# Performance work log

Hardware: AMD Instinct MI355X
Metric: run time of the kernel (lower is better)

Reference implementation:

```python
import jax, jax.numpy as jnp
import numpy as np

GROUPS = 32
EPS = 1e-5
HEAD_DIM = 64


def group_norm(x, gamma, beta):
    # x: [B, L, C]; normalize over (L, C//G) within each of G channel groups
    B, L, C = x.shape
    g = x.reshape(B, L, GROUPS, C // GROUPS)
    mean = g.mean(axis=(1, 3), keepdims=True)
    var = g.var(axis=(1, 3), keepdims=True)
    g = (g - mean) * jax.lax.rsqrt(var + EPS)
    return g.reshape(B, L, C) * gamma + beta


def setup_inputs() -> dict:
    key = jax.random.key(0)
    ks = jax.random.split(key, 4)
    B, H, W, C = 16, 32, 32, 512
    x = jax.random.normal(ks[0], (B, H, W, C), dtype=jnp.float32)
    timesteps = jax.random.randint(ks[1], (B,), 0, 1000)
    gamma = jnp.ones((C,), jnp.float32)
    beta = jnp.zeros((C,), jnp.float32)
    w_qkv = jax.random.normal(ks[2], (C, 3 * C), dtype=jnp.float32) * (1.0 / np.sqrt(C))
    b_qkv = jnp.zeros((3 * C,), jnp.float32)
    w_out = jax.random.normal(ks[3], (C, C), dtype=jnp.float32) * (1.0 / np.sqrt(C))
    b_out = jnp.zeros((C,), jnp.float32)
    return {"x": x, "timesteps": timesteps, "gamma": gamma, "beta": beta,
            "w_qkv": w_qkv, "b_qkv": b_qkv, "w_out": w_out, "b_out": b_out}


def reference(x, timesteps, gamma, beta, w_qkv, b_qkv, w_out, b_out):
    B, H, W, C = x.shape
    L = H * W
    nh = C // HEAD_DIM
    factor = jnp.asarray(1.0 / np.sqrt(np.sqrt(HEAD_DIM)), x.dtype)  # applied to both q and k

    xf = x.reshape(B, L, C)
    qkv = group_norm(xf, gamma, beta) @ w_qkv + b_qkv        # [B, L, 3C]
    q, k, v = jnp.split(qkv, 3, axis=-1)

    def heads(t):  # [B, L, C] -> [B, nh, L, d]
        return t.reshape(B, L, nh, HEAD_DIM).transpose(0, 2, 1, 3)

    q, k, v = heads(q) * factor, heads(k) * factor, heads(v)
    scores = jnp.einsum('bhqd,bhkd->bhqk', q, k)             # [B, nh, L, L]
    attn = jax.nn.softmax(scores, axis=-1)
    out = jnp.einsum('bhqk,bhkd->bhqd', attn, v)             # [B, nh, L, d]
    out = out.transpose(0, 2, 1, 3).reshape(B, L, C)
    h = out @ w_out + b_out
    return (xf + h).reshape(B, H, W, C)
```

## Files before the change

### kernel.cpp

```cpp
#include <hip/hip_runtime.h>

#define Bn 16
#define Ln 1024
#define Cn 512
#define Mn (Bn*Ln)
#define N3n 1536

typedef unsigned short u16;
typedef __attribute__((ext_vector_type(8))) short short8;
typedef __attribute__((ext_vector_type(4))) float f32x4;
typedef __attribute__((ext_vector_type(16))) float f32x16;

typedef const __attribute__((address_space(1))) void* gas_p;
typedef __attribute__((address_space(3))) void* las_p;

__device__ inline void gl_lds16(const void* g, void* l) {
  __builtin_amdgcn_global_load_lds((gas_p)g, (las_p)l, 16, 0, 0);
}

__device__ inline u16 f2bf(float f) {
  union { float f; unsigned u; } v; v.f = f;
  unsigned r = v.u + 0x7FFFu + ((v.u >> 16) & 1u);
  return (u16)(r >> 16);
}

__device__ inline unsigned pk2(float a, float b) {
  return (__float_as_uint(a) >> 16) | (__float_as_uint(b) & 0xFFFF0000u);
}

__device__ inline f32x4 mfma16(short8 a, short8 b, f32x4 c) {
  return __builtin_amdgcn_mfma_f32_16x16x32_bf16(a, b, c, 0, 0, 0);
}
__device__ inline f32x16 mfma32(short8 a, short8 b, f32x16 c) {
  return __builtin_amdgcn_mfma_f32_32x32x16_bf16(a, b, c, 0, 0, 0);
}

__global__ __launch_bounds__(256) void k_gn(const float* __restrict__ x,
                                            const float* __restrict__ gamma,
                                            const float* __restrict__ beta,
                                            u16* __restrict__ gn) {
  __shared__ __attribute__((aligned(16))) float xs[1024 * 16];
  __shared__ float red[8];
  __shared__ float stat[2];
  int bid = blockIdx.x;
  int b = bid >> 5, g = bid & 31;
  const float* base = x + (size_t)b * (Ln * Cn) + g * 16;
  int tid = threadIdx.x;
  int c = tid & 3;
  float s1 = 0.f, s2 = 0.f;
  for (int i = 0; i < 16; ++i) {
    int s = i * 256 + tid;
    int r = s >> 2;
    float4 v = *(const float4*)(base + (size_t)r * Cn + c * 4);
    *(float4*)(xs + (size_t)s * 4) = v;
    s1 += v.x + v.y + v.z + v.w;
    s2 += v.x * v.x + v.y * v.y + v.z * v.z + v.w * v.w;
  }
  s1 += __shfl_xor(s1, 1);  s2 += __shfl_xor(s2, 1);
  s1 += __shfl_xor(s1, 2);  s2 += __shfl_xor(s2, 2);
  s1 += __shfl_xor(s1, 4);  s2 += __shfl_xor(s2, 4);
  s1 += __shfl_xor(s1, 8);  s2 += __shfl_xor(s2, 8);
  s1 += __shfl_xor(s1, 16); s2 += __shfl_xor(s2, 16);
  s1 += __shfl_xor(s1, 32); s2 += __shfl_xor(s2, 32);
  int w = tid >> 6, lane = tid & 63;
  if (lane == 0) { red[w] = s1; red[4 + w] = s2; }
  __syncthreads();
  if (tid == 0) {
    float a = red[0] + red[1] + red[2] + red[3];
    float q = red[4] + red[5] + red[6] + red[7];
    float mean = a * (1.f / 16384.f);
    float var = q * (1.f / 16384.f) - mean * mean;
    stat[0] = mean;
    stat[1] = rsqrtf(var + 1e-5f);
  }
  __syncthreads();
  float mean = stat[0], rstd = stat[1];
  float4 gv = *(const float4*)(gamma + g * 16 + c * 4);
  float4 bv = *(const float4*)(beta + g * 16 + c * 4);
  u16* gdst = gn + (size_t)b * (Ln * Cn) + g * 16;
  for (int i = 0; i < 16; ++i) {
    int s = i * 256 + tid;
    int r = s >> 2;
    float4 v = *(const float4*)(xs + (size_t)s * 4);
    ushort4 o;
    o.x = f2bf((v.x - mean) * rstd * gv.x + bv.x);
    o.y = f2bf((v.y - mean) * rstd * gv.y + bv.y);
    o.z = f2bf((v.z - mean) * rstd * gv.z + bv.z);
    o.w = f2bf((v.w - mean) * rstd * gv.w + bv.w);
    *(ushort4*)(gdst + (size_t)r * Cn + c * 4) = o;
  }
}

__global__ __launch_bounds__(256) void k_wtrans(const float* __restrict__ wqkv,
                                                const float* __restrict__ wout,
                                                u16* __restrict__ wqkvT,
                                                u16* __restrict__ woutT) {
  __shared__ float T[64][65];
  int bid = blockIdx.x;
  const float* src; u16* dst; int srcN, k0, n0;
  if (bid < 192) {
    src = wqkv; dst = wqkvT; srcN = 1536;
    int nt = bid % 24, kt = bid / 24;
    n0 = nt * 64; k0 = kt * 64;
  } else {
    int b2 = bid - 192;
    src = wout; dst = woutT; srcN = 512;
    int nt = b2 & 7, kt = b2 >> 3;
    n0 = nt * 64; k0 = kt * 64;
  }
  int tid = threadIdx.x;
  int r = tid >> 4, c4 = tid & 15;
#pragma unroll
  for (int i = 0; i < 4; ++i) {
    int rr = i * 16 + r;
    float4 v = *(const float4*)(src + (size_t)(k0 + rr) * srcN + n0 + c4 * 4);
    T[rr][c4 * 4 + 0] = v.x; T[rr][c4 * 4 + 1] = v.y;
    T[rr][c4 * 4 + 2] = v.z; T[rr][c4 * 4 + 3] = v.w;
  }
  __syncthreads();
  int r2 = tid >> 3, c2 = tid & 7;
#pragma unroll
  for (int i = 0; i < 2; ++i) {
    int nn = i * 32 + r2;
    int kk = c2 * 8;
    uint4 pk;
    pk.x = (unsigned)f2bf(T[kk + 0][nn]) | ((unsigned)f2bf(T[kk + 1][nn]) << 16);
    pk.y = (unsigned)f2bf(T[kk + 2][nn]) | ((unsigned)f2bf(T[kk + 3][nn]) << 16);
    pk.z = (unsigned)f2bf(T[kk + 4][nn]) | ((unsigned)f2bf(T[kk + 5][nn]) << 16);
    pk.w = (unsigned)f2bf(T[kk + 6][nn]) | ((unsigned)f2bf(T[kk + 7][nn]) << 16);
    *(uint4*)(dst + (size_t)(n0 + nn) * 512 + k0 + kk) = pk;
  }
}

__global__ __launch_bounds__(256) void k_qkv(const u16* __restrict__ gn,
                                             const u16* __restrict__ wT,
                                             const float* __restrict__ bias,
                                             u16* __restrict__ qb,
                                             u16* __restrict__ kb,
                                             u16* __restrict__ vT) {
  __shared__ __attribute__((aligned(16))) char smem[66560];
  int bid = blockIdx.x;
  int wg = (bid & 7) * 192 + (bid >> 3);
  int tn = wg % 12, tm = wg / 12;
  int m0 = tm * 128, n0 = tn * 128;
  int tid = threadIdx.x;
  int w = tid >> 6, lane = tid & 63, lr = lane & 15, lg = lane >> 4;
  int wr = w >> 1, wc = w & 1;
  const f32x4 fzero = {0.f, 0.f, 0.f, 0.f};
  f32x4 acc[4][4];
#pragma unroll
  for (int mi = 0; mi < 4; ++mi)
#pragma unroll
    for (int ni = 0; ni < 4; ++ni) acc[mi][ni] = fzero;

#pragma unroll
  for (int i = 0; i < 4; ++i) {
    int s = i * 256 + tid;
    int r = s >> 3, c = s & 7;
    gl_lds16(gn + ((size_t)(m0 + r) * 512 + ((c ^ (r & 7)) << 3)),
             smem + ((s & ~63) << 4));
    gl_lds16(wT + ((size_t)(n0 + r) * 512 + ((c ^ (r & 7)) << 3)),
             smem + 32768 + ((s & ~63) << 4));
  }
  __syncthreads();

  for (int kt = 0; kt < 8; ++kt) {
    int cur = kt & 1;
    char* Asb = smem + cur * 16384;
    char* Bsb = smem + 32768 + cur * 16384;
    if (kt < 7) {
      int nb = cur ^ 1, k0n = (kt + 1) * 64;
#pragma unroll
      for (int i = 0; i < 4; ++i) {
        int s = i * 256 + tid;
        int r = s >> 3, c = s & 7;
        gl_lds16(gn + ((size_t)(m0 + r) * 512 + k0n + ((c ^ (r & 7)) << 3)),
                 smem + nb * 16384 + ((s & ~63) << 4));
        gl_lds16(wT + ((size_t)(n0 + r) * 512 + k0n + ((c ^ (r & 7)) << 3)),
                 smem + 32768 + nb * 16384 + ((s & ~63) << 4));
      }
    }
#pragma unroll
    for (int ks = 0; ks < 2; ++ks) {
      short8 af[4], bf[4];
#pragma unroll
      for (int mi = 0; mi < 4; ++mi) {
        int row = wr * 64 + mi * 16 + lr;
        int ck = ks * 4 + lg;
        af[mi] = *(const short8*)(Asb + row * 128 + ((ck ^ (lr & 7)) << 4));
      }
#pragma unroll
      for (int ni = 0; ni < 4; ++ni) {
        int row = wc * 64 + ni * 16 + lr;
        int ck = ks * 4 + lg;
        bf[ni] = *(const short8*)(Bsb + row * 128 + ((ck ^ (lr & 7)) << 4));
      }
#pragma unroll
      for (int mi = 0; mi < 4; ++mi)
#pragma unroll
        for (int ni = 0; ni < 4; ++ni)
          acc[mi][ni] = mfma16(af[mi], bf[ni], acc[mi][ni]);
    }
    __syncthreads();
  }

  if (tn >= 8) {
    float* T = (float*)smem;
#pragma unroll
    for (int mi = 0; mi < 4; ++mi)
#pragma unroll
      for (int ni = 0; ni < 4; ++ni) {
        int n_l = wc * 64 + ni * 16 + lr;
        float bn = bias[n0 + n_l];
#pragma unroll
        for (int rr = 0; rr < 4; ++rr) {
          int m_l = wr * 64 + mi * 16 + lg * 4 + rr;
          T[n_l * 130 + m_l] = acc[mi][ni][rr] + bn;
        }
      }
    __syncthreads();
    int n_l = tid >> 1, half = tid & 1;
    int nv = n0 - 1024 + n_l;
    int h = nv >> 6, dd = nv & 63;
    int bb = m0 >> 10, li0 = m0 & 1023;
    u16* dst = vT + ((size_t)(bb * 8 + h) * 64 + dd) * 1024 + li0;
    const float* Tr = T + n_l * 130;
#pragma unroll
    for (int j = 0; j < 8; ++j) {
      int mb = half * 8 + 16 * j;
#define SIG(IDX) (((IDX) & ~15) | (((IDX) & 4) << 1) | (((IDX) & 8) >> 1) | ((IDX) & 3))
      uint4 o;
      o.x = (unsigned)f2bf(Tr[SIG(mb + 0)]) | ((unsigned)f2bf(Tr[SIG(mb + 1)]) << 16);
      o.y = (unsigned)f2bf(Tr[SIG(mb + 2)]) | ((unsigned)f2bf(Tr[SIG(mb + 3)]) << 16);
      o.z = (unsigned)f2bf(Tr[SIG(mb + 4)]) | ((unsigned)f2bf(Tr[SIG(mb + 5)]) << 16);
      o.w = (unsigned)f2bf(Tr[SIG(mb + 6)]) | ((unsigned)f2bf(Tr[SIG(mb + 7)]) << 16);
#undef SIG
      *(uint4*)(dst + mb) = o;
    }
  } else {
    const float C1 = 0.18033688011112042f;
#pragma unroll
    for (int mi = 0; mi < 4; ++mi) {
#pragma unroll
      for (int ni = 0; ni < 4; ++ni) {
        int n = n0 + wc * 64 + ni * 16 + lr;
        float bn = bias[n];
        int which = n >> 9, nn = n & 511;
        int h = nn >> 6, dd = nn & 63;
#pragma unroll
        for (int rr = 0; rr < 4; ++rr) {
          int m = m0 + wr * 64 + mi * 16 + lg * 4 + rr;
          float v = acc[mi][ni][rr] + bn;
          int bb = m >> 10, li = m & 1023;
          if (which == 0)
            qb[((size_t)(bb * 8 + h) * 1024 + li) * 64 + dd] = f2bf(v * C1);
          else
            kb[((size_t)(bb * 8 + h) * 1024 + li) * 64 + dd] = f2bf(v);
        }
      }
    }
  }
}

__global__ __launch_bounds__(512, 4) void k_attn(const u16* __restrict__ qb,
                                                 const u16* __restrict__ kb,
                                                 const u16* __restrict__ vT,
                                                 u16* __restrict__ ob) {
  __shared__ __attribute__((aligned(16))) u16 Ks[3 * 64 * 64];
  __shared__ __attribute__((aligned(16))) u16 Vs[3 * 64 * 64];
  int bid = blockIdx.x;
  int xq = bid & 7, kk = bid >> 3;
  int bh = ((kk & 15) << 3) | xq;
  int qt = kk >> 4;
  const u16* qh = qb + (size_t)bh * 65536;
  const u16* kh = kb + (size_t)bh * 65536;
  const u16* vh = vT + (size_t)bh * 65536;
  int tid = threadIdx.x, w = tid >> 6, lane = tid & 63;
  int l31 = lane & 31, lhi = lane >> 5;
  int q0 = qt * 256 + w * 32;

  short8 qf[4];
#pragma unroll
  for (int ks = 0; ks < 4; ++ks)
    qf[ks] = *(const short8*)(qh + (size_t)(q0 + l31) * 64 + ks * 16 + lhi * 8);

  f32x16 accO[2];
#pragma unroll
  for (int dt = 0; dt < 2; ++dt)
#pragma unroll
    for (int r = 0; r < 16; ++r) accO[dt][r] = 0.f;
  float lst = 0.f;

  int sr = tid >> 3, sc8 = tid & 7;
  size_t koff = (size_t)sr * 64 + ((sc8 ^ (sr & 7)) << 3);
  size_t voff = (size_t)sr * 1024 + ((sc8 ^ (sr & 7)) << 3);
  int ldst = (tid & ~63) << 4;

  gl_lds16(kh + koff, (char*)Ks + ldst);
  gl_lds16(vh + voff, (char*)Vs + ldst);
  gl_lds16(kh + 4096 + koff, (char*)Ks + 8192 + ldst);
  gl_lds16(vh + 64 + voff, (char*)Vs + 8192 + ldst);
  asm volatile("s_waitcnt vmcnt(2)" ::: "memory");
  __builtin_amdgcn_s_barrier();

#pragma unroll 1
  for (int jt = 0; jt < 16; ++jt) {
    int cb = jt % 3;
    char* Ksb = (char*)Ks + cb * 8192;
    char* Vsb = (char*)Vs + cb * 8192;
    if (jt < 14) {
      int nb = (jt + 2) % 3;
      gl_lds16(kh + (size_t)(jt + 2) * 4096 + koff, (char*)Ks + nb * 8192 + ldst);
      gl_lds16(vh + (size_t)(jt + 2) * 64 + voff, (char*)Vs + nb * 8192 + ldst);
    }

    f32x16 sc0, sc1;
#pragma unroll
    for (int r = 0; r < 16; ++r) { sc0[r] = 0.f; sc1[r] = 0.f; }
#pragma unroll
    for (int ks = 0; ks < 4; ++ks) {
      int row = l31;
      short8 kf = *(const short8*)(Ksb + row * 128 + (((2 * ks + lhi) ^ (row & 7)) << 4));
      sc0 = mfma32(kf, qf[ks], sc0);
    }
#pragma unroll
    for (int ks = 0; ks < 4; ++ks) {
      int row = 32 + l31;
      short8 kf = *(const short8*)(Ksb + row * 128 + (((2 * ks + lhi) ^ (row & 7)) << 4));
      sc1 = mfma32(kf, qf[ks], sc1);
    }

    float rs = 0.f;
#pragma unroll
    for (int r = 0; r < 16; ++r) {
      float pp = __builtin_amdgcn_exp2f(sc0[r]);
      sc0[r] = pp; rs += pp;
    }
#pragma unroll
    for (int r = 0; r < 16; ++r) {
      float pp = __builtin_amdgcn_exp2f(sc1[r]);
      sc1[r] = pp; rs += pp;
    }
    lst += rs;

    short8 ap[4];
    {
      union { uint4 u; short8 s; } cv;
      cv.u.x = pk2(sc0[0], sc0[1]);  cv.u.y = pk2(sc0[2], sc0[3]);
      cv.u.z = pk2(sc0[4], sc0[5]);  cv.u.w = pk2(sc0[6], sc0[7]);
      ap[0] = cv.s;
      cv.u.x = pk2(sc0[8], sc0[9]);  cv.u.y = pk2(sc0[10], sc0[11]);
      cv.u.z = pk2(sc0[12], sc0[13]); cv.u.w = pk2(sc0[14], sc0[15]);
      ap[1] = cv.s;
      cv.u.x = pk2(sc1[0], sc1[1]);  cv.u.y = pk2(sc1[2], sc1[3]);
      cv.u.z = pk2(sc1[4], sc1[5]);  cv.u.w = pk2(sc1[6], sc1[7]);
      ap[2] = cv.s;
      cv.u.x = pk2(sc1[8], sc1[9]);  cv.u.y = pk2(sc1[10], sc1[11]);
      cv.u.z = pk2(sc1[12], sc1[13]); cv.u.w = pk2(sc1[14], sc1[15]);
      ap[3] = cv.s;
    }

#pragma unroll
    for (int ks2 = 0; ks2 < 4; ++ks2) {
#pragma unroll
      for (int dt = 0; dt < 2; ++dt) {
        int row = dt * 32 + l31;
        short8 bv = *(const short8*)(Vsb + row * 128 + (((2 * ks2 + lhi) ^ (row & 7)) << 4));
        accO[dt] = mfma32(ap[ks2], bv, accO[dt]);
      }
    }

    if (jt < 14)
      asm volatile("s_waitcnt vmcnt(2)" ::: "memory");
    else
      asm volatile("s_waitcnt vmcnt(0)" ::: "memory");
    __builtin_amdgcn_s_barrier();
  }

  int b = bh >> 3, h = bh & 7;
  float lt = lst + __shfl_xor(lst, 32);
  float il = 1.f / lt;
#pragma unroll
  for (int reg = 0; reg < 16; ++reg) {
    int qrow = (reg & 3) + 8 * (reg >> 2) + 4 * lhi;
    float ib = __shfl(il, qrow);
    int row = q0 + qrow;
#pragma unroll
    for (int dt = 0; dt < 2; ++dt) {
      int col = h * 64 + dt * 32 + l31;
      ob[(size_t)(b * 1024 + row) * 512 + col] = f2bf(accO[dt][reg] * ib);
    }
  }
}

__global__ __launch_bounds__(256) void k_out(const u16* __restrict__ ob,
                                             const u16* __restrict__ wT,
                                             const float* __restrict__ bias,
                                             const float* __restrict__ x,
                                             float* __restrict__ out) {
  __shared__ __attribute__((aligned(16))) u16 As[2 * 128 * 64];
  __shared__ __attribute__((aligned(16))) u16 Bs[2 * 128 * 64];
  int bid = blockIdx.x;
  int wg = (bid & 7) * 64 + (bid >> 3);
  int tn = wg & 3, tm = wg >> 2;
  int m0 = tm * 128, n0 = tn * 128;
  int tid = threadIdx.x;
  int w = tid >> 6, lane = tid & 63, lr = lane & 15, lg = lane >> 4;
  int wr = w >> 1, wc = w & 1;
  const f32x4 fzero = {0.f, 0.f, 0.f, 0.f};
  f32x4 acc[4][4];
#pragma unroll
  for (int mi = 0; mi < 4; ++mi)
#pragma unroll
    for (int ni = 0; ni < 4; ++ni) acc[mi][ni] = fzero;

#pragma unroll
  for (int i = 0; i < 4; ++i) {
    int s = i * 256 + tid;
    int r = s >> 3, c = s & 7;
    gl_lds16(ob + ((size_t)(m0 + r) * 512 + ((c ^ (r & 7)) << 3)),
             (char*)As + ((s & ~63) << 4));
    gl_lds16(wT + ((size_t)(n0 + r) * 512 + ((c ^ (r & 7)) << 3)),
             (char*)Bs + ((s & ~63) << 4));
  }
  __syncthreads();

  for (int kt = 0; kt < 8; ++kt) {
    int cur = kt & 1;
    char* Asb = (char*)As + cur * 16384;
    char* Bsb = (char*)Bs + cur * 16384;
    if (kt < 7) {
      int nb = cur ^ 1, k0n = (kt + 1) * 64;
#pragma unroll
      for (int i = 0; i < 4; ++i) {
        int s = i * 256 + tid;
        int r = s >> 3, c = s & 7;
        gl_lds16(ob + ((size_t)(m0 + r) * 512 + k0n + ((c ^ (r & 7)) << 3)),
                 (char*)As + nb * 16384 + ((s & ~63) << 4));
        gl_lds16(wT + ((size_t)(n0 + r) * 512 + k0n + ((c ^ (r & 7)) << 3)),
                 (char*)Bs + nb * 16384 + ((s & ~63) << 4));
      }
    }
#pragma unroll
    for (int ks = 0; ks < 2; ++ks) {
      short8 af[4], bf[4];
#pragma unroll
      for (int mi = 0; mi < 4; ++mi) {
        int row = wr * 64 + mi * 16 + lr;
        int ck = ks * 4 + lg;
        af[mi] = *(const short8*)(Asb + row * 128 + ((ck ^ (lr & 7)) << 4));
      }
#pragma unroll
      for (int ni = 0; ni < 4; ++ni) {
        int row = wc * 64 + ni * 16 + lr;
        int ck = ks * 4 + lg;
        bf[ni] = *(const short8*)(Bsb + row * 128 + ((ck ^ (lr & 7)) << 4));
      }
#pragma unroll
      for (int mi = 0; mi < 4; ++mi)
#pragma unroll
        for (int ni = 0; ni < 4; ++ni)
          acc[mi][ni] = mfma16(af[mi], bf[ni], acc[mi][ni]);
    }
    __syncthreads();
  }
#pragma unroll
  for (int mi = 0; mi < 4; ++mi) {
#pragma unroll
    for (int ni = 0; ni < 4; ++ni) {
      int n = n0 + wc * 64 + ni * 16 + lr;
      float bn = bias[n];
#pragma unroll
      for (int rr = 0; rr < 4; ++rr) {
        int m = m0 + wr * 64 + mi * 16 + lg * 4 + rr;
        size_t off = (size_t)m * 512 + n;
        out[off] = x[off] + acc[mi][ni][rr] + bn;
      }
    }
  }
}

extern "C" void kernel_launch(void* const* d_in, const int* in_sizes, int n_in,
                              void* d_out, int out_size, void* d_ws, size_t ws_size,
                              hipStream_t stream) {
  const float* x = (const float*)d_in[0];
  const float* gamma = (const float*)d_in[2];
  const float* beta = (const float*)d_in[3];
  const float* wqkv = (const float*)d_in[4];
  const float* bqkv = (const float*)d_in[5];
  const float* wout = (const float*)d_in[6];
  const float* bout = (const float*)d_in[7];
  float* out = (float*)d_out;

  char* ws = (char*)d_ws;
  u16* gn = (u16*)(ws + 4096);
  u16* wqkvT = (u16*)(ws + 4096 + 16777216);
  u16* woutT = (u16*)(ws + 4096 + 16777216 + 1572864);
  u16* qb = (u16*)(ws + 4096 + 16777216 + 1572864 + 524288);
  u16* kb = qb + 8388608;
  u16* vT = kb + 8388608;
  u16* ob = vT + 8388608;

  k_gn<<<512, 256, 0, stream>>>(x, gamma, beta, gn);
  k_wtrans<<<256, 256, 0, stream>>>(wqkv, wout, wqkvT, woutT);
  k_qkv<<<1536, 256, 0, stream>>>(gn, wqkvT, bqkv, qb, kb, vT);
  k_attn<<<512, 512, 0, stream>>>(qb, kb, vT, ob);
  k_out<<<512, 256, 0, stream>>>(ob, woutT, bout, x, out);
}
```

Baseline: 116.9 us.

## Use four-stage 32-wide K pipeline with explicit vmcnt waits in QKV GEMM

Restructures the QKV projection GEMM main loop from a double-buffered 64-wide K step into a four-slot ring of 32-wide K tiles with two tiles in flight. It replaces __syncthreads with explicit s_waitcnt vmcnt plus s_barrier so loads for later stages stay outstanding across iterations. The LDS swizzle is changed to fit the 64-byte rows. The goal is to hide global-to-LDS latency better, at the cost of twice as many iterations and barriers and hand-managed wait counts that must match the number of loads issued.

```diff
diff --git a/kernel.cpp b/kernel.cpp
--- a/kernel.cpp
+++ b/kernel.cpp
@@ -153,56 +153,61 @@
 #pragma unroll
     for (int ni = 0; ni < 4; ++ni) acc[mi][ni] = fzero;
 
-#pragma unroll
-  for (int i = 0; i < 4; ++i) {
-    int s = i * 256 + tid;
-    int r = s >> 3, c = s & 7;
-    gl_lds16(gn + ((size_t)(m0 + r) * 512 + ((c ^ (r & 7)) << 3)),
-             smem + ((s & ~63) << 4));
-    gl_lds16(wT + ((size_t)(n0 + r) * 512 + ((c ^ (r & 7)) << 3)),
-             smem + 32768 + ((s & ~63) << 4));
-  }
-  __syncthreads();
-
-  for (int kt = 0; kt < 8; ++kt) {
-    int cur = kt & 1;
-    char* Asb = smem + cur * 16384;
-    char* Bsb = smem + 32768 + cur * 16384;
-    if (kt < 7) {
-      int nb = cur ^ 1, k0n = (kt + 1) * 64;
-#pragma unroll
-      for (int i = 0; i < 4; ++i) {
-        int s = i * 256 + tid;
-        int r = s >> 3, c = s & 7;
-        gl_lds16(gn + ((size_t)(m0 + r) * 512 + k0n + ((c ^ (r & 7)) << 3)),
-                 smem + nb * 16384 + ((s & ~63) << 4));
-        gl_lds16(wT + ((size_t)(n0 + r) * 512 + k0n + ((c ^ (r & 7)) << 3)),
-                 smem + 32768 + nb * 16384 + ((s & ~63) << 4));
-      }
-    }
-#pragma unroll
-    for (int ks = 0; ks < 2; ++ks) {
-      short8 af[4], bf[4];
-#pragma unroll
-      for (int mi = 0; mi < 4; ++mi) {
-        int row = wr * 64 + mi * 16 + lr;
-        int ck = ks * 4 + lg;
-        af[mi] = *(const short8*)(Asb + row * 128 + ((ck ^ (lr & 7)) << 4));
-      }
-#pragma unroll
-      for (int ni = 0; ni < 4; ++ni) {
-        int row = wc * 64 + ni * 16 + lr;
-        int ck = ks * 4 + lg;
-        bf[ni] = *(const short8*)(Bsb + row * 128 + ((ck ^ (lr & 7)) << 4));
-      }
-#pragma unroll
-      for (int mi = 0; mi < 4; ++mi)
-#pragma unroll
-        for (int ni = 0; ni < 4; ++ni)
-          acc[mi][ni] = mfma16(af[mi], bf[ni], acc[mi][ni]);
-    }
-    __syncthreads();
-  }
+  int s0 = tid, s1a = 256 + tid;
+  int r0 = s0 >> 2, c0 = s0 & 3, r1 = s1a >> 2, c1 = s1a & 3;
+  size_t ga0 = (size_t)(m0 + r0) * 512 + ((c0 ^ ((r0 >> 1) & 3)) << 3);
+  size_t ga1 = (size_t)(m0 + r1) * 512 + ((c1 ^ ((r1 >> 1) & 3)) << 3);
+  size_t gb0 = (size_t)(n0 + r0) * 512 + ((c0 ^ ((r0 >> 1) & 3)) << 3);
+  size_t gb1 = (size_t)(n0 + r1) * 512 + ((c1 ^ ((r1 >> 1) & 3)) << 3);
+  int ld0 = (s0 & ~63) << 4;
+  int ld1 = (s1a & ~63) << 4;
+
+#define STAGE(KT)                                                              \
+  {                                                                            \
+    char* Ab = smem + (((KT) & 3) * 8192);                                     \
+    char* Bb = smem + 32768 + (((KT) & 3) * 8192);                             \
+    int ko = (KT) * 32;                                                        \
+    gl_lds16(gn + ga0 + ko, Ab + ld0);                                         \
+    gl_lds16(gn + ga1 + ko, Ab + ld1);                                         \
+    gl_lds16(wT + gb0 + ko, Bb + ld0);                                         \
+    gl_lds16(wT + gb1 + ko, Bb + ld1);                                         \
+  }
+
+  STAGE(0)
+  STAGE(1)
+  asm volatile("s_waitcnt vmcnt(4)" ::: "memory");
+  __builtin_amdgcn_s_barrier();
+
+#pragma unroll 1
+  for (int kt = 0; kt < 16; ++kt) {
+    char* Asb = smem + ((kt & 3) * 8192);
+    char* Bsb = smem + 32768 + ((kt & 3) * 8192);
+    if (kt < 14) STAGE(kt + 2)
+
+    short8 af[4], bf[4];
+#pragma unroll
+    for (int mi = 0; mi < 4; ++mi) {
+      int row = wr * 64 + mi * 16 + lr;
+      af[mi] = *(const short8*)(Asb + row * 64 + ((lg ^ ((row >> 1) & 3)) << 4));
+    }
+#pragma unroll
+    for (int ni = 0; ni < 4; ++ni) {
+      int row = wc * 64 + ni * 16 + lr;
+      bf[ni] = *(const short8*)(Bsb + row * 64 + ((lg ^ ((row >> 1) & 3)) << 4));
+    }
+#pragma unroll
+    for (int mi = 0; mi < 4; ++mi)
+#pragma unroll
+      for (int ni = 0; ni < 4; ++ni)
+        acc[mi][ni] = mfma16(af[mi], bf[ni], acc[mi][ni]);
+
+    if (kt < 14)
+      asm volatile("s_waitcnt vmcnt(4)" ::: "memory");
+    else
+      asm volatile("s_waitcnt vmcnt(0)" ::: "memory");
+    __builtin_amdgcn_s_barrier();
+  }
+#undef STAGE
 
   if (tn >= 8) {
     float* T = (float*)smem;
```

Result: slower. 122.6 us (+4.9%).

## Single-buffer QKV GEMM tiles and split V transpose to halve LDS use

Applied to the files above, without the earlier changes.

Drops double buffering of the A/B tiles in the QKV GEMM, so each k-step now loads, syncs and then computes. The V-transpose epilogue is split into two 64-column passes so its staging buffer fits in the smaller shared allocation. Shared memory drops from about 65KB to 33KB per block, which can allow more resident blocks per CU. In exchange, global loads no longer overlap with the MFMA compute inside a block, and the epilogue gains extra barriers.

```diff
diff --git a/kernel.cpp b/kernel.cpp
--- a/kernel.cpp
+++ b/kernel.cpp
@@ -138,7 +138,7 @@
                                              u16* __restrict__ qb,
                                              u16* __restrict__ kb,
                                              u16* __restrict__ vT) {
-  __shared__ __attribute__((aligned(16))) char smem[66560];
+  __shared__ __attribute__((aligned(16))) char smem[33280];
   int bid = blockIdx.x;
   int wg = (bid & 7) * 192 + (bid >> 3);
   int tn = wg % 12, tm = wg / 12;
@@ -153,33 +153,21 @@
 #pragma unroll
     for (int ni = 0; ni < 4; ++ni) acc[mi][ni] = fzero;
 
-#pragma unroll
-  for (int i = 0; i < 4; ++i) {
-    int s = i * 256 + tid;
-    int r = s >> 3, c = s & 7;
-    gl_lds16(gn + ((size_t)(m0 + r) * 512 + ((c ^ (r & 7)) << 3)),
-             smem + ((s & ~63) << 4));
-    gl_lds16(wT + ((size_t)(n0 + r) * 512 + ((c ^ (r & 7)) << 3)),
-             smem + 32768 + ((s & ~63) << 4));
-  }
-  __syncthreads();
+  char* Asb = smem;
+  char* Bsb = smem + 16384;
 
   for (int kt = 0; kt < 8; ++kt) {
-    int cur = kt & 1;
-    char* Asb = smem + cur * 16384;
-    char* Bsb = smem + 32768 + cur * 16384;
-    if (kt < 7) {
-      int nb = cur ^ 1, k0n = (kt + 1) * 64;
-#pragma unroll
-      for (int i = 0; i < 4; ++i) {
-        int s = i * 256 + tid;
-        int r = s >> 3, c = s & 7;
-        gl_lds16(gn + ((size_t)(m0 + r) * 512 + k0n + ((c ^ (r & 7)) << 3)),
-                 smem + nb * 16384 + ((s & ~63) << 4));
-        gl_lds16(wT + ((size_t)(n0 + r) * 512 + k0n + ((c ^ (r & 7)) << 3)),
-                 smem + 32768 + nb * 16384 + ((s & ~63) << 4));
-      }
-    }
+    int k0 = kt * 64;
+#pragma unroll
+    for (int i = 0; i < 4; ++i) {
+      int s = i * 256 + tid;
+      int r = s >> 3, c = s & 7;
+      gl_lds16(gn + ((size_t)(m0 + r) * 512 + k0 + ((c ^ (r & 7)) << 3)),
+               Asb + ((s & ~63) << 4));
+      gl_lds16(wT + ((size_t)(n0 + r) * 512 + k0 + ((c ^ (r & 7)) << 3)),
+               Bsb + ((s & ~63) << 4));
+    }
+    __syncthreads();
 #pragma unroll
     for (int ks = 0; ks < 2; ++ks) {
       short8 af[4], bf[4];
@@ -205,37 +193,43 @@
   }
 
   if (tn >= 8) {
-    float* T = (float*)smem;
-#pragma unroll
-    for (int mi = 0; mi < 4; ++mi)
-#pragma unroll
-      for (int ni = 0; ni < 4; ++ni) {
-        int n_l = wc * 64 + ni * 16 + lr;
-        float bn = bias[n0 + n_l];
-#pragma unroll
-        for (int rr = 0; rr < 4; ++rr) {
-          int m_l = wr * 64 + mi * 16 + lg * 4 + rr;
-          T[n_l * 130 + m_l] = acc[mi][ni][rr] + bn;
-        }
-      }
-    __syncthreads();
-    int n_l = tid >> 1, half = tid & 1;
-    int nv = n0 - 1024 + n_l;
-    int h = nv >> 6, dd = nv & 63;
+    float* T2 = (float*)smem;
     int bb = m0 >> 10, li0 = m0 & 1023;
-    u16* dst = vT + ((size_t)(bb * 8 + h) * 64 + dd) * 1024 + li0;
-    const float* Tr = T + n_l * 130;
-#pragma unroll
-    for (int j = 0; j < 8; ++j) {
-      int mb = half * 8 + 16 * j;
+    int r2 = tid >> 2, qd = tid & 3;
+#pragma unroll
+    for (int h0 = 0; h0 < 2; ++h0) {
+      if (wc == h0) {
+#pragma unroll
+        for (int mi = 0; mi < 4; ++mi)
+#pragma unroll
+          for (int ni = 0; ni < 4; ++ni) {
+            int nl2 = ni * 16 + lr;
+            float bn = bias[n0 + h0 * 64 + nl2];
+#pragma unroll
+            for (int rr = 0; rr < 4; ++rr) {
+              int m_l = wr * 64 + mi * 16 + lg * 4 + rr;
+              T2[nl2 * 130 + m_l] = acc[mi][ni][rr] + bn;
+            }
+          }
+      }
+      __syncthreads();
+      int nv = n0 - 1024 + h0 * 64 + r2;
+      int h = nv >> 6, dd = nv & 63;
+      u16* dst = vT + ((size_t)(bb * 8 + h) * 64 + dd) * 1024 + li0;
+      const float* Tr = T2 + r2 * 130;
+#pragma unroll
+      for (int j = 0; j < 4; ++j) {
+        int mb = qd * 8 + j * 32;
 #define SIG(IDX) (((IDX) & ~15) | (((IDX) & 4) << 1) | (((IDX) & 8) >> 1) | ((IDX) & 3))
-      uint4 o;
-      o.x = (unsigned)f2bf(Tr[SIG(mb + 0)]) | ((unsigned)f2bf(Tr[SIG(mb + 1)]) << 16);
-      o.y = (unsigned)f2bf(Tr[SIG(mb + 2)]) | ((unsigned)f2bf(Tr[SIG(mb + 3)]) << 16);
-      o.z = (unsigned)f2bf(Tr[SIG(mb + 4)]) | ((unsigned)f2bf(Tr[SIG(mb + 5)]) << 16);
-      o.w = (unsigned)f2bf(Tr[SIG(mb + 6)]) | ((unsigned)f2bf(Tr[SIG(mb + 7)]) << 16);
+        uint4 o;
+        o.x = (unsigned)f2bf(Tr[SIG(mb + 0)]) | ((unsigned)f2bf(Tr[SIG(mb + 1)]) << 16);
+        o.y = (unsigned)f2bf(Tr[SIG(mb + 2)]) | ((unsigned)f2bf(Tr[SIG(mb + 3)]) << 16);
+        o.z = (unsigned)f2bf(Tr[SIG(mb + 4)]) | ((unsigned)f2bf(Tr[SIG(mb + 5)]) << 16);
+        o.w = (unsigned)f2bf(Tr[SIG(mb + 6)]) | ((unsigned)f2bf(Tr[SIG(mb + 7)]) << 16);
 #undef SIG
-      *(uint4*)(dst + mb) = o;
+        *(uint4*)(dst + mb) = o;
+      }
+      __syncthreads();
     }
   } else {
     const float C1 = 0.18033688011112042f;
```

Measured after the change: 125.2 us. 1.07x slower.
